# Performance work log

Hardware: AMD Instinct MI355X
Metric: run time of the kernel (lower is better)

## Reference

```python
import jax, jax.numpy as jnp
import numpy as np
from jax.scipy.special import logsumexp

B, T, V, E, H, C, L = 128, 1024, 21, 32, 100, 20, 2


def setup_inputs() -> dict:
    key = jax.random.key(0)
    ks = jax.random.split(key, 32)
    def n(i, shape, scale=0.1):
        return (jax.random.normal(ks[i], shape) * scale).astype(jnp.float32)
    inp = {}
    inp["tokens"] = jax.random.randint(ks[0], (B, T), 0, V)
    inp["seq_lengths"] = jnp.full((B,), T, dtype=jnp.int32)
    inp["emb"] = n(1, (V, E), 1.0)
    idx = 2
    for l in range(L):
        din = E if l == 0 else 2 * H
        for sfx in ["", "_rev"]:
            inp[f"W_ih_l{l}{sfx}"] = n(idx, (4 * H, din)); idx += 1
            inp[f"W_hh_l{l}{sfx}"] = n(idx, (4 * H, H)); idx += 1
            inp[f"b_ih_l{l}{sfx}"] = n(idx, (4 * H,)); idx += 1
            inp[f"b_hh_l{l}{sfx}"] = n(idx, (4 * H,)); idx += 1
    inp["fW"] = n(idx, (C, 2 * H)); idx += 1
    inp["fb"] = n(idx, (C,)); idx += 1
    inp["gW"] = n(idx, (C * C, 2 * H)); idx += 1
    inp["gb"] = n(idx, (C * C,)); idx += 1
    inp["h0"] = n(idx, (2 * L, B, H), 1.0); idx += 1
    inp["c0"] = n(idx, (2 * L, B, H), 1.0)
    return inp


def _lstm_dir(x, Wih, Whh, bih, bhh, h0, c0, reverse):
    # x: [B,T,D]; precompute input projection once (PyTorch gate order i,f,g,o)
    xp = jnp.einsum('btd,gd->btg', x, Wih) + bih + bhh  # [B,T,4H]
    def step(carry, xt):
        h, c = carry
        gates = xt + h @ Whh.T
        i, f, g, o = jnp.split(gates, 4, axis=-1)
        c = jax.nn.sigmoid(f) * c + jax.nn.sigmoid(i) * jnp.tanh(g)
        h = jax.nn.sigmoid(o) * jnp.tanh(c)
        return (h, c), h
    _, hs = jax.lax.scan(step, (h0, c0), jnp.swapaxes(xp, 0, 1), reverse=reverse)
    return jnp.swapaxes(hs, 0, 1)  # [B,T,H]


def _crf_alpha(f, g):
    # alpha[0]=f[0]; alpha[t]=f[t]+LSE_i(alpha[t-1,i]+g[t,i,:])
    fs = jnp.swapaxes(f, 0, 1)  # [T,B,C]
    gs = jnp.swapaxes(g, 0, 1)  # [T,B,C,C]
    def step(a, fg):
        ft, gt = fg
        a = ft + logsumexp(a[:, :, None] + gt, axis=1)
        return a, a
    _, alphas = jax.lax.scan(step, fs[0], (fs[1:], gs[1:]))
    return jnp.swapaxes(jnp.concatenate([fs[:1], alphas], 0), 0, 1)


def _crf_beta(f, g):
    # beta[T-1]=0; beta[t]=LSE_j(g[t+1,:,j]+f[t+1,j]+beta[t+1,j])
    fs = jnp.swapaxes(f, 0, 1)
    gs = jnp.swapaxes(g, 0, 1)
    def step(b, fg):
        fnx, gnx = fg
        b = logsumexp(gnx + (fnx + b)[:, None, :], axis=2)
        return b, b
    bT = jnp.zeros_like(fs[0])
    _, betas = jax.lax.scan(step, bT, (fs[1:], gs[1:]), reverse=True)
    return jnp.swapaxes(jnp.concatenate([betas, bT[None]], 0), 0, 1)


def reference(tokens, seq_lengths, emb,
              W_ih_l0, W_hh_l0, b_ih_l0, b_hh_l0,
              W_ih_l0_rev, W_hh_l0_rev, b_ih_l0_rev, b_hh_l0_rev,
              W_ih_l1, W_hh_l1, b_ih_l1, b_hh_l1,
              W_ih_l1_rev, W_hh_l1_rev, b_ih_l1_rev, b_hh_l1_rev,
              fW, fb, gW, gb, h0, c0):
    x = emb[tokens]  # [B,T,E]
    # layer 0 (bidirectional)
    of = _lstm_dir(x, W_ih_l0, W_hh_l0, b_ih_l0, b_hh_l0, h0[0], c0[0], False)
    ob = _lstm_dir(x, W_ih_l0_rev, W_hh_l0_rev, b_ih_l0_rev, b_hh_l0_rev, h0[1], c0[1], True)
    x1 = jnp.concatenate([of, ob], axis=-1)  # dropout between layers: eval mode (identity)
    # layer 1
    of = _lstm_dir(x1, W_ih_l1, W_hh_l1, b_ih_l1, b_hh_l1, h0[2], c0[2], False)
    ob = _lstm_dir(x1, W_ih_l1_rev, W_hh_l1_rev, b_ih_l1_rev, b_hh_l1_rev, h0[3], c0[3], True)
    h = jnp.concatenate([of, ob], axis=-1)  # [B,T,2H]
    # pad_packed_sequence zeroes positions beyond seq_lengths
    mask = (jnp.arange(T)[None, :] < seq_lengths[:, None]).astype(h.dtype)
    h = h * mask[:, :, None]
    f_out = h @ fW.T + fb                      # [B,T,C] emissions
    g_out = (h @ gW.T + gb).reshape(B, T, C, C)  # [B,T,C,C] transitions
    alpha = _crf_alpha(f_out, g_out)
    beta = _crf_beta(f_out, g_out)
    logZ = logsumexp(alpha[:, -1], axis=-1)    # [B]
    log_marg = alpha + beta - logZ[:, None, None]
    return (jnp.exp(log_marg), f_out, g_out, alpha, beta)
```

## Files before the change

### kernel.cpp

```cpp
#include <hip/hip_runtime.h>
#include <hip/hip_bf16.h>

#define B_ 128
#define T_ 1024
#define E_ 32
#define H_ 100
#define C_ 20
#define M_ (B_*T_)

typedef __attribute__((ext_vector_type(8))) short bf16x8v;
typedef __attribute__((ext_vector_type(4))) float f32x4v;
typedef __attribute__((ext_vector_type(2))) _Float16 h2v;
typedef unsigned short u16;
typedef unsigned int u32;

static __device__ __forceinline__ short f2b(float x) {
  union { __hip_bfloat16 b; short s; } u;
  u.b = __float2bfloat16(x);
  return u.s;
}
static __device__ __forceinline__ float b2f(u16 x) {
  return __uint_as_float(((u32)x) << 16);
}

#if __has_builtin(__builtin_amdgcn_fdot2)
#define FDOT2(w, p, c) __builtin_amdgcn_fdot2((w), (p), (c), false)
#else
static __device__ __forceinline__ float FDOT2(h2v w, h2v p, float c) {
  return fmaf((float)w[1], (float)p[1], fmaf((float)w[0], (float)p[0], c));
}
#endif

__global__ void embed_k(const int* __restrict__ tok, const float* __restrict__ emb,
                        float* __restrict__ x0) {
  int idx = blockIdx.x * 256 + threadIdx.x;
  int bt = idx >> 5;
  int e  = idx & 31;
  x0[idx] = emb[tok[bt] * E_ + e];
}

template<int ABF, int OBF>
__global__ __launch_bounds__(256) void gemm_mfma_t(
    const void* __restrict__ Av, const float* __restrict__ W,
    const float* __restrict__ b1, const float* __restrict__ b2,
    void* __restrict__ Cv, int K, int N, int ldc)
{
  __shared__ short as[64 * 40];
  __shared__ short ws[64 * 40];
  const float* Af = (const float*)Av;
  const u16*   Ab = (const u16*)Av;
  float* Cf = (float*)Cv;
  u16*   Cb = (u16*)Cv;
  int tid = threadIdx.x, lane = tid & 63, w = tid >> 6;
  int lr = lane & 15, lq = lane >> 4;
  size_t m0 = (size_t)blockIdx.x * 64;
  int n0 = blockIdx.y * 64;
  int srow = tid >> 2;
  int sk = (tid & 3) * 8;
  bool wok = (n0 + srow) < N;
  const float* Wp = wok ? (W + (size_t)(n0 + srow) * K + sk) : W;
  size_t arow = (m0 + srow) * (size_t)K;
  f32x4v acc[4];
  #pragma unroll
  for (int r = 0; r < 4; ++r) acc[r] = (f32x4v){0.f, 0.f, 0.f, 0.f};
  int ksteps = (K + 31) / 32;
  for (int ks = 0; ks < ksteps; ++ks) {
    int kk = ks * 32;
    bf16x8v av, wv;
    if (kk + sk + 7 < K) {
      if (ABF) {
        av = *(const bf16x8v*)(Ab + arow + kk + sk);
      } else {
        float4 a0 = *(const float4*)(Af + arow + kk + sk);
        float4 a1 = *(const float4*)(Af + arow + kk + sk + 4);
        av[0]=f2b(a0.x); av[1]=f2b(a0.y); av[2]=f2b(a0.z); av[3]=f2b(a0.w);
        av[4]=f2b(a1.x); av[5]=f2b(a1.y); av[6]=f2b(a1.z); av[7]=f2b(a1.w);
      }
      if (wok) {
        float4 w0 = *(const float4*)(Wp + kk);
        float4 w1 = *(const float4*)(Wp + kk + 4);
        wv[0]=f2b(w0.x); wv[1]=f2b(w0.y); wv[2]=f2b(w0.z); wv[3]=f2b(w0.w);
        wv[4]=f2b(w1.x); wv[5]=f2b(w1.y); wv[6]=f2b(w1.z); wv[7]=f2b(w1.w);
      } else {
        #pragma unroll
        for (int j = 0; j < 8; ++j) wv[j] = 0;
      }
    } else {
      #pragma unroll
      for (int j = 0; j < 8; ++j) {
        int k = kk + sk + j;
        av[j] = (k < K) ? (ABF ? (short)Ab[arow + k] : f2b(Af[arow + k])) : (short)0;
        wv[j] = (wok && k < K) ? f2b(W[(size_t)(n0 + srow) * K + k]) : (short)0;
      }
    }
    *(bf16x8v*)&as[srow * 40 + sk] = av;
    *(bf16x8v*)&ws[srow * 40 + sk] = wv;
    __syncthreads();
    bf16x8v bf = *(const bf16x8v*)&ws[(16 * w + lr) * 40 + 8 * lq];
    #pragma unroll
    for (int r = 0; r < 4; ++r) {
      bf16x8v af = *(const bf16x8v*)&as[(16 * r + lr) * 40 + 8 * lq];
      acc[r] = __builtin_amdgcn_mfma_f32_16x16x32_bf16(af, bf, acc[r], 0, 0, 0);
    }
    __syncthreads();
  }
  int col = n0 + 16 * w + lr;
  if (col < N) {
    float bv = (b1 ? b1[col] : 0.f) + (b2 ? b2[col] : 0.f);
    #pragma unroll
    for (int r = 0; r < 4; ++r)
      #pragma unroll
      for (int rg = 0; rg < 4; ++rg) {
        size_t off = (m0 + 16 * r + 4 * lq + rg) * (size_t)ldc + col;
        float v = acc[r][rg] + bv;
        if (OBF) Cb[off] = (u16)f2b(v); else Cf[off] = v;
      }
  }
}

__global__ __launch_bounds__(256, 1) void lstm_scan(
    const u16* __restrict__ xp,
    const float* __restrict__ WhhF, const float* __restrict__ WhhR,
    const float* __restrict__ h0, const float* __restrict__ c0,
    const int* __restrict__ seqlen,
    u16* __restrict__ outbuf,
    int layer)
{
  int wg = blockIdx.x; int dir = wg & 1; int b = wg >> 1;
  int tid = threadIdx.x;
  const float* Whh = dir ? WhhR : WhhF;
  const u16* xpp = xp + ((size_t)dir * B_ + b) * T_ * 400;
  const float* h0p = h0 + ((size_t)(2 * layer + dir) * B_ + b) * H_;
  const float* c0p = c0 + ((size_t)(2 * layer + dir) * B_ + b) * H_;
  __shared__ __align__(16) float gsh[400];
  __shared__ __align__(16) _Float16 hph[112];
  bool act = (tid < 200);
  u32 w0p[52], w1p[52];
  if (act) {
    const float* r0 = Whh + (size_t)(2 * tid) * H_;
    const float* r1 = Whh + (size_t)(2 * tid + 1) * H_;
    #pragma unroll
    for (int j = 0; j < 52; ++j) {
      float a0 = (j < 50) ? r0[2 * j] : 0.f;
      float a1 = (j < 50) ? r0[2 * j + 1] : 0.f;
      float c0v = (j < 50) ? r1[2 * j] : 0.f;
      float c1v = (j < 50) ? r1[2 * j + 1] : 0.f;
      w0p[j] = __builtin_bit_cast(u32, (h2v){(_Float16)a0, (_Float16)a1});
      w1p[j] = __builtin_bit_cast(u32, (h2v){(_Float16)c0v, (_Float16)c1v});
    }
    #pragma unroll
    for (int j = 0; j < 52; ++j)
      asm volatile("" : "+v"(w0p[j]), "+v"(w1p[j]));
  }
  if (tid < 112) hph[tid] = (_Float16)((tid < H_) ? h0p[tid] : 0.f);
  float c = (tid < H_) ? c0p[tid] : 0.f;
  int sl = seqlen ? seqlen[b] : T_;
  __syncthreads();
  int tstep = dir ? -1 : 1;
  int t0 = dir ? (T_ - 1) : 0;
  ushort2 xc = make_ushort2(0, 0), xn = make_ushort2(0, 0);
  if (act) {
    xc = *(const ushort2*)(xpp + (size_t)t0 * 400 + 2 * tid);
    xn = *(const ushort2*)(xpp + (size_t)(t0 + tstep) * 400 + 2 * tid);
  }
  for (int tt = 0; tt < T_; ++tt) {
    int t = t0 + tstep * tt;
    ushort2 xn2 = make_ushort2(0, 0);
    if (act && tt + 2 < T_)
      xn2 = *(const ushort2*)(xpp + (size_t)(t + 2 * tstep) * 400 + 2 * tid);
    if (act) {
      float a0 = b2f(xc.x), a1 = b2f(xc.y);
      #pragma unroll
      for (int q = 0; q < 13; ++q) {
        f32x4v hp = ((const f32x4v*)hph)[q];
        #pragma unroll
        for (int i = 0; i < 4; ++i) {
          h2v p = __builtin_bit_cast(h2v, hp[i]);
          a0 = FDOT2(__builtin_bit_cast(h2v, w0p[4 * q + i]), p, a0);
          a1 = FDOT2(__builtin_bit_cast(h2v, w1p[4 * q + i]), p, a1);
        }
      }
      *(float2*)&gsh[2 * tid] = make_float2(a0, a1);
    }
    __syncthreads();
    if (tid < H_) {
      float gi = gsh[tid], gf = gsh[H_ + tid], gg = gsh[2 * H_ + tid], go = gsh[3 * H_ + tid];
      float si = 1.f / (1.f + __expf(-gi));
      float sf = 1.f / (1.f + __expf(-gf));
      float so = 1.f / (1.f + __expf(-go));
      float tg = 1.f - 2.f / (1.f + __expf(2.f * gg));
      c = fmaf(sf, c, si * tg);
      float tc = 1.f - 2.f / (1.f + __expf(2.f * c));
      float h = so * tc;
      hph[tid] = (_Float16)h;
      outbuf[((size_t)b * T_ + t) * 200 + dir * H_ + tid] = (t < sl) ? (u16)f2b(h) : (u16)0;
    }
    __syncthreads();
    xc = xn; xn = xn2;
  }
}

__global__ __launch_bounds__(64) void crf_k(
    const float* __restrict__ f, const float* __restrict__ g,
    float* __restrict__ alpha, float* __restrict__ beta)
{
  int wg = blockIdx.x;
  int lane = threadIdx.x;
  float gv[20], gn1[20], gn2[20], sv[20];
  #pragma unroll
  for (int q = 0; q < 20; ++q) { gv[q] = 0.f; gn1[q] = 0.f; gn2[q] = 0.f; }
  if (wg < B_) {
    int b = wg;
    const float* fp = f + (size_t)b * T_ * C_;
    const float* gp = g + (size_t)b * T_ * C_ * C_;
    float* ap = alpha + (size_t)b * T_ * C_;
    float a = 0.f;
    if (lane < C_) { a = fp[lane]; ap[lane] = a; }
    if (lane < C_) {
      #pragma unroll
      for (int q = 0; q < 20; ++q) gv[q] = gp[(size_t)1 * 400 + q * 20 + lane];
      #pragma unroll
      for (int q = 0; q < 20; ++q) gn1[q] = gp[(size_t)2 * 400 + q * 20 + lane];
    }
    for (int t = 1; t < T_; ++t) {
      if (t + 2 < T_ && lane < C_) {
        #pragma unroll
        for (int q = 0; q < 20; ++q) gn2[q] = gp[(size_t)(t + 2) * 400 + q * 20 + lane];
      }
      float ft = (lane < C_) ? fp[t * C_ + lane] : 0.f;
      float m = -3.0e38f;
      #pragma unroll
      for (int q = 0; q < 20; ++q) {
        float s = __shfl(a, q) + gv[q];
        sv[q] = s; m = fmaxf(m, s);
      }
      float sum = 0.f;
      #pragma unroll
      for (int q = 0; q < 20; ++q) sum += __expf(sv[q] - m);
      a = ft + m + __logf(sum);
      if (lane < C_) ap[(size_t)t * C_ + lane] = a;
      #pragma unroll
      for (int q = 0; q < 20; ++q) { gv[q] = gn1[q]; gn1[q] = gn2[q]; }
    }
  } else {
    int b = wg - B_;
    const float* fp = f + (size_t)b * T_ * C_;
    const float* gp = g + (size_t)b * T_ * C_ * C_;
    float* bp = beta + (size_t)b * T_ * C_;
    float bv = 0.f;
    if (lane < C_) bp[(size_t)(T_ - 1) * C_ + lane] = 0.f;
    if (lane < C_) {
      #pragma unroll
      for (int q = 0; q < 20; ++q) gv[q] = gp[(size_t)(T_ - 1) * 400 + lane * 20 + q];
      #pragma unroll
      for (int q = 0; q < 20; ++q) gn1[q] = gp[(size_t)(T_ - 2) * 400 + lane * 20 + q];
    }
    for (int t = T_ - 2; t >= 0; --t) {
      if (t >= 2 && lane < C_) {
        #pragma unroll
        for (int q = 0; q < 20; ++q) gn2[q] = gp[(size_t)(t - 1) * 400 + lane * 20 + q];
      }
      float w = ((lane < C_) ? fp[(t + 1) * C_ + lane] : 0.f) + bv;
      float m = -3.0e38f;
      #pragma unroll
      for (int q = 0; q < 20; ++q) {
        float s = gv[q] + __shfl(w, q);
        sv[q] = s; m = fmaxf(m, s);
      }
      float sum = 0.f;
      #pragma unroll
      for (int q = 0; q < 20; ++q) sum += __expf(sv[q] - m);
      bv = m + __logf(sum);
      if (lane < C_) bp[(size_t)t * C_ + lane] = bv;
      #pragma unroll
      for (int q = 0; q < 20; ++q) { gv[q] = gn1[q]; gn1[q] = gn2[q]; }
    }
  }
}

__global__ void logz_k(const float* __restrict__ alpha, float* __restrict__ lz) {
  int b = blockIdx.x; int lane = threadIdx.x;
  float a = (lane < C_) ? alpha[((size_t)b * T_ + (T_ - 1)) * C_ + lane] : -3.0e38f;
  float m = a;
  #pragma unroll
  for (int o = 32; o > 0; o >>= 1) m = fmaxf(m, __shfl_xor(m, o));
  float e = (lane < C_) ? __expf(a - m) : 0.f;
  #pragma unroll
  for (int o = 32; o > 0; o >>= 1) e += __shfl_xor(e, o);
  if (lane == 0) lz[b] = m + __logf(e);
}

__global__ void marg_k(const float* __restrict__ alpha, const float* __restrict__ beta,
                       const float* __restrict__ lz, float* __restrict__ out0) {
  size_t idx = (size_t)blockIdx.x * 256 + threadIdx.x;
  int b = (int)(idx / (T_ * C_));
  out0[idx] = __expf(alpha[idx] + beta[idx] - lz[b]);
}

extern "C" void kernel_launch(void* const* d_in, const int* in_sizes, int n_in,
                              void* d_out, int out_size, void* d_ws, size_t ws_size,
                              hipStream_t stream) {
  const int*   tok   = (const int*)d_in[0];
  const int*   seq   = (const int*)d_in[1];
  const float* emb   = (const float*)d_in[2];
  const float* Wih0  = (const float*)d_in[3];
  const float* Whh0  = (const float*)d_in[4];
  const float* bih0  = (const float*)d_in[5];
  const float* bhh0  = (const float*)d_in[6];
  const float* Wih0r = (const float*)d_in[7];
  const float* Whh0r = (const float*)d_in[8];
  const float* bih0r = (const float*)d_in[9];
  const float* bhh0r = (const float*)d_in[10];
  const float* Wih1  = (const float*)d_in[11];
  const float* Whh1  = (const float*)d_in[12];
  const float* bih1  = (const float*)d_in[13];
  const float* bhh1  = (const float*)d_in[14];
  const float* Wih1r = (const float*)d_in[15];
  const float* Whh1r = (const float*)d_in[16];
  const float* bih1r = (const float*)d_in[17];
  const float* bhh1r = (const float*)d_in[18];
  const float* fW    = (const float*)d_in[19];
  const float* fb    = (const float*)d_in[20];
  const float* gW    = (const float*)d_in[21];
  const float* gb    = (const float*)d_in[22];
  const float* h0    = (const float*)d_in[23];
  const float* c0    = (const float*)d_in[24];

  float* ws = (float*)d_ws;
  float* x0  = ws;
  u16*   xp  = (u16*)(ws + 4194304);
  u16*   x1  = (u16*)(ws + 109051904);
  float* lz  = ws + 135266304;

  float* out   = (float*)d_out;
  float* f_out = out + 2621440;
  float* g_out = out + 5242880;
  float* a_out = out + 57671680;
  float* b_out = out + 60293120;

  embed_k<<<16384, 256, 0, stream>>>(tok, emb, x0);

  dim3 g400(2048, 7), g20(2048, 1);
  gemm_mfma_t<0,1><<<g400, 256, 0, stream>>>(x0, Wih0,  bih0,  bhh0,  xp,                    32, 400, 400);
  gemm_mfma_t<0,1><<<g400, 256, 0, stream>>>(x0, Wih0r, bih0r, bhh0r, xp + (size_t)52428800, 32, 400, 400);
  lstm_scan<<<256, 256, 0, stream>>>(xp, Whh0, Whh0r, h0, c0, nullptr, x1, 0);
  gemm_mfma_t<1,1><<<g400, 256, 0, stream>>>(x1, Wih1,  bih1,  bhh1,  xp,                    200, 400, 400);
  gemm_mfma_t<1,1><<<g400, 256, 0, stream>>>(x1, Wih1r, bih1r, bhh1r, xp + (size_t)52428800, 200, 400, 400);
  lstm_scan<<<256, 256, 0, stream>>>(xp, Whh1, Whh1r, h0, c0, seq, x1, 1);
  gemm_mfma_t<1,0><<<g20,  256, 0, stream>>>(x1, fW, fb, nullptr, f_out, 200, 20,  20);
  gemm_mfma_t<1,0><<<g400, 256, 0, stream>>>(x1, gW, gb, nullptr, g_out, 200, 400, 400);
  crf_k<<<256, 64, 0, stream>>>(f_out, g_out, a_out, b_out);
  logz_k<<<128, 64, 0, stream>>>(a_out, lz);
  marg_k<<<10240, 256, 0, stream>>>(a_out, b_out, lz, out);
}
```

Baseline: 3.042 ms.

## Stage CRF transition tiles through an LDS ring buffer with coalesced float4 prefetch

The alpha and beta CRF recurrences now load each 400-float transition block with coalesced float4 reads spread over 50 lanes. The blocks go into a 4-deep shared-memory ring buffer, with register prefetch running three steps ahead. The alpha and beta state is broadcast through shared memory instead of lane shuffles, and the max and exp-sum reductions use tree form for more instruction-level parallelism. This is meant to cut the strided per-lane global loads (especially the row-strided beta access) and the shuffle latency on the serial critical path. It relies on single-wavefront lockstep ordering and has no explicit barriers.

```diff
diff --git a/kernel.cpp b/kernel.cpp
--- a/kernel.cpp
+++ b/kernel.cpp
@@ -206,74 +206,135 @@
 {
   int wg = blockIdx.x;
   int lane = threadIdx.x;
-  float gv[20], gn1[20], gn2[20], sv[20];
-  #pragma unroll
-  for (int q = 0; q < 20; ++q) { gv[q] = 0.f; gn1[q] = 0.f; gn2[q] = 0.f; }
+  __shared__ __align__(16) float gl[4][400];
+  __shared__ __align__(16) float aw[20];
+  bool stv = lane < 50;
+  int p0 = 8 * lane;
+  float4 rA0, rA1, rB0, rB1;
+
   if (wg < B_) {
     int b = wg;
     const float* fp = f + (size_t)b * T_ * C_;
     const float* gp = g + (size_t)b * T_ * C_ * C_;
     float* ap = alpha + (size_t)b * T_ * C_;
-    float a = 0.f;
-    if (lane < C_) { a = fp[lane]; ap[lane] = a; }
     if (lane < C_) {
-      #pragma unroll
-      for (int q = 0; q < 20; ++q) gv[q] = gp[(size_t)1 * 400 + q * 20 + lane];
-      #pragma unroll
-      for (int q = 0; q < 20; ++q) gn1[q] = gp[(size_t)2 * 400 + q * 20 + lane];
+      float a0 = fp[lane];
+      ap[lane] = a0;
+      aw[lane] = a0;
+    }
+    if (stv) {
+      float4 v0 = *(const float4*)(gp + 400 + p0);
+      float4 v1 = *(const float4*)(gp + 404 + p0);
+      *(float4*)&gl[1 & 3][p0] = v0;  *(float4*)&gl[1 & 3][p0 + 4] = v1;
+      v0 = *(const float4*)(gp + 800 + p0);
+      v1 = *(const float4*)(gp + 804 + p0);
+      *(float4*)&gl[2 & 3][p0] = v0;  *(float4*)&gl[2 & 3][p0 + 4] = v1;
+      rA0 = *(const float4*)(gp + 1200 + p0);
+      rA1 = *(const float4*)(gp + 1204 + p0);
     }
     for (int t = 1; t < T_; ++t) {
-      if (t + 2 < T_ && lane < C_) {
-        #pragma unroll
-        for (int q = 0; q < 20; ++q) gn2[q] = gp[(size_t)(t + 2) * 400 + q * 20 + lane];
-      }
-      float ft = (lane < C_) ? fp[t * C_ + lane] : 0.f;
-      float m = -3.0e38f;
-      #pragma unroll
-      for (int q = 0; q < 20; ++q) {
-        float s = __shfl(a, q) + gv[q];
-        sv[q] = s; m = fmaxf(m, s);
-      }
-      float sum = 0.f;
-      #pragma unroll
-      for (int q = 0; q < 20; ++q) sum += __expf(sv[q] - m);
-      a = ft + m + __logf(sum);
-      if (lane < C_) ap[(size_t)t * C_ + lane] = a;
-      #pragma unroll
-      for (int q = 0; q < 20; ++q) { gv[q] = gn1[q]; gn1[q] = gn2[q]; }
+      if (stv && (t + 3 < T_)) {
+        rB0 = *(const float4*)(gp + (size_t)(t + 3) * 400 + p0);
+        rB1 = *(const float4*)(gp + (size_t)(t + 3) * 400 + p0 + 4);
+      }
+      if (lane < C_) {
+        const float* gr = &gl[t & 3][0];
+        float ft = fp[(size_t)t * C_ + lane];
+        float awv[20];
+        #pragma unroll
+        for (int q = 0; q < 5; ++q)
+          *(f32x4v*)&awv[4 * q] = ((const f32x4v*)aw)[q];
+        float s[20];
+        #pragma unroll
+        for (int i = 0; i < 20; ++i)
+          s[i] = awv[i] + gr[i * 20 + lane];
+        float m4[5];
+        #pragma unroll
+        for (int q = 0; q < 5; ++q)
+          m4[q] = fmaxf(fmaxf(s[4*q], s[4*q+1]), fmaxf(s[4*q+2], s[4*q+3]));
+        float m = fmaxf(fmaxf(m4[0], m4[1]), fmaxf(fmaxf(m4[2], m4[3]), m4[4]));
+        float e4[5];
+        #pragma unroll
+        for (int q = 0; q < 5; ++q) {
+          float e0 = __expf(s[4*q] - m),   e1 = __expf(s[4*q+1] - m);
+          float e2 = __expf(s[4*q+2] - m), e3 = __expf(s[4*q+3] - m);
+          e4[q] = (e0 + e1) + (e2 + e3);
+        }
+        float sum = (e4[0] + e4[1]) + ((e4[2] + e4[3]) + e4[4]);
+        float an = ft + m + __logf(sum);
+        ap[(size_t)t * C_ + lane] = an;
+        aw[lane] = an;
+      }
+      if (stv && (t + 2 < T_)) {
+        *(float4*)&gl[(t + 2) & 3][p0] = rA0;
+        *(float4*)&gl[(t + 2) & 3][p0 + 4] = rA1;
+      }
+      rA0 = rB0; rA1 = rB1;
     }
   } else {
     int b = wg - B_;
     const float* fp = f + (size_t)b * T_ * C_;
     const float* gp = g + (size_t)b * T_ * C_ * C_;
     float* bp = beta + (size_t)b * T_ * C_;
-    float bv = 0.f;
-    if (lane < C_) bp[(size_t)(T_ - 1) * C_ + lane] = 0.f;
     if (lane < C_) {
-      #pragma unroll
-      for (int q = 0; q < 20; ++q) gv[q] = gp[(size_t)(T_ - 1) * 400 + lane * 20 + q];
-      #pragma unroll
-      for (int q = 0; q < 20; ++q) gn1[q] = gp[(size_t)(T_ - 2) * 400 + lane * 20 + q];
-    }
-    for (int t = T_ - 2; t >= 0; --t) {
-      if (t >= 2 && lane < C_) {
-        #pragma unroll
-        for (int q = 0; q < 20; ++q) gn2[q] = gp[(size_t)(t - 1) * 400 + lane * 20 + q];
-      }
-      float w = ((lane < C_) ? fp[(t + 1) * C_ + lane] : 0.f) + bv;
-      float m = -3.0e38f;
-      #pragma unroll
-      for (int q = 0; q < 20; ++q) {
-        float s = gv[q] + __shfl(w, q);
-        sv[q] = s; m = fmaxf(m, s);
-      }
-      float sum = 0.f;
-      #pragma unroll
-      for (int q = 0; q < 20; ++q) sum += __expf(sv[q] - m);
-      bv = m + __logf(sum);
-      if (lane < C_) bp[(size_t)t * C_ + lane] = bv;
-      #pragma unroll
-      for (int q = 0; q < 20; ++q) { gv[q] = gn1[q]; gn1[q] = gn2[q]; }
+      bp[(size_t)(T_ - 1) * C_ + lane] = 0.f;
+      aw[lane] = fp[(size_t)(T_ - 1) * C_ + lane];
+    }
+    if (stv) {
+      float4 v0 = *(const float4*)(gp + (size_t)(T_ - 1) * 400 + p0);
+      float4 v1 = *(const float4*)(gp + (size_t)(T_ - 1) * 400 + p0 + 4);
+      *(float4*)&gl[(T_ - 1) & 3][p0] = v0;  *(float4*)&gl[(T_ - 1) & 3][p0 + 4] = v1;
+      v0 = *(const float4*)(gp + (size_t)(T_ - 2) * 400 + p0);
+      v1 = *(const float4*)(gp + (size_t)(T_ - 2) * 400 + p0 + 4);
+      *(float4*)&gl[(T_ - 2) & 3][p0] = v0;  *(float4*)&gl[(T_ - 2) & 3][p0 + 4] = v1;
+      rA0 = *(const float4*)(gp + (size_t)(T_ - 3) * 400 + p0);
+      rA1 = *(const float4*)(gp + (size_t)(T_ - 3) * 400 + p0 + 4);
+    }
+    for (int u = 1; u < T_; ++u) {
+      int t = T_ - 1 - u;
+      int r = t + 1;
+      if (stv && (r - 3 >= 1)) {
+        rB0 = *(const float4*)(gp + (size_t)(r - 3) * 400 + p0);
+        rB1 = *(const float4*)(gp + (size_t)(r - 3) * 400 + p0 + 4);
+      }
+      if (lane < C_) {
+        const float* gr = &gl[r & 3][lane * 20];
+        float fcur = fp[(size_t)t * C_ + lane];
+        float awv[20];
+        #pragma unroll
+        for (int q = 0; q < 5; ++q)
+          *(f32x4v*)&awv[4 * q] = ((const f32x4v*)aw)[q];
+        float s[20];
+        #pragma unroll
+        for (int q = 0; q < 5; ++q) {
+          f32x4v gq = *(const f32x4v*)&gr[4 * q];
+          s[4*q]   = awv[4*q]   + gq[0];
+          s[4*q+1] = awv[4*q+1] + gq[1];
+          s[4*q+2] = awv[4*q+2] + gq[2];
+          s[4*q+3] = awv[4*q+3] + gq[3];
+        }
+        float m4[5];
+        #pragma unroll
+        for (int q = 0; q < 5; ++q)
+          m4[q] = fmaxf(fmaxf(s[4*q], s[4*q+1]), fmaxf(s[4*q+2], s[4*q+3]));
+        float m = fmaxf(fmaxf(m4[0], m4[1]), fmaxf(fmaxf(m4[2], m4[3]), m4[4]));
+        float e4[5];
+        #pragma unroll
+        for (int q = 0; q < 5; ++q) {
+          float e0 = __expf(s[4*q] - m),   e1 = __expf(s[4*q+1] - m);
+          float e2 = __expf(s[4*q+2] - m), e3 = __expf(s[4*q+3] - m);
+          e4[q] = (e0 + e1) + (e2 + e3);
+        }
+        float sum = (e4[0] + e4[1]) + ((e4[2] + e4[3]) + e4[4]);
+        float bn = m + __logf(sum);
+        bp[(size_t)t * C_ + lane] = bn;
+        aw[lane] = fcur + bn;
+      }
+      if (stv && (r - 2 >= 1)) {
+        *(float4*)&gl[(r - 2) & 3][p0] = rA0;
+        *(float4*)&gl[(r - 2) & 3][p0 + 4] = rA1;
+      }
+      rA0 = rB0; rA1 = rB1;
     }
   }
 }
```

After: 2.739 ms. 1.11x faster.
